# Kernel tuning notes

Measured on AMD Instinct MI355X. Metric: run time of the kernel, lower is better.

The kernel has to match this reference:

```python
import jax, jax.numpy as jnp
import numpy as np

GAMMA = 9.6
BETA = 0.83
LAMDA = 10.0
EPS = 1e-12

B, D, C = 1024, 512, 10000


def _l2norm(x):
    # torch F.normalize: x / max(||x||_2, eps)
    n = jnp.sqrt(jnp.sum(x * x, axis=1, keepdims=True))
    return x / jnp.maximum(n, EPS)


def setup_inputs() -> dict:
    key = jax.random.key(0)
    k1, k2, k3, k4 = jax.random.split(key, 4)
    inp = jax.random.normal(k1, (B, D), dtype=jnp.float32)
    # xavier-uniform-like init for the classifier weight
    limit = float(np.sqrt(6.0 / (C + D)))
    weight = jax.random.uniform(k2, (C, D), dtype=jnp.float32, minval=-limit, maxval=limit)
    class_weight = jax.random.uniform(k3, (C,), dtype=jnp.float32)  # per-class margins in [0,1)
    label = jax.random.randint(k4, (B,), 0, C, dtype=jnp.int32)
    return {"input": inp, "weight": weight, "class_weight": class_weight, "label": label}


def reference(input, weight, class_weight, label):
    x = _l2norm(input)            # [B, D]
    w = _l2norm(weight)           # [C, D]
    fea = x @ w.T                 # [B, C] cosine logits

    # sp_i = fea[i, label_i]; logit_{ij} = sn_ij - sp_i + beta * m_j  (j != label_i)
    sp = jnp.take_along_axis(fea, label[:, None], axis=1)           # [B, 1]
    logits = GAMMA * (fea - sp + BETA * class_weight[None, :])      # [B, C]
    pos_mask = label[:, None] == jnp.arange(C, dtype=label.dtype)[None, :]
    logits = jnp.where(pos_mask, -jnp.inf, logits)                  # drop positive column
    lse = jax.scipy.special.logsumexp(logits, axis=1)               # [B]
    loss = jax.nn.softplus(lse)                                     # [B]

    # inter-class similarity penalty
    score = jnp.clip(w @ w.T, -1.0, 1.0)                            # [C, C]
    score = score * (1.0 - jnp.eye(C, dtype=score.dtype))           # zero diagonal
    s = jnp.max(score[label], axis=1)                               # [B]
    loss_w = jax.nn.softplus(jnp.mean(s) + 0.5)

    loss = loss + LAMDA * loss_w
    return fea, jnp.mean(loss)
```

## Files before the change

### kernel.cpp

```cpp
#include <hip/hip_runtime.h>
#include <math.h>

#define GAMMA 9.6f
#define BETA  0.83f
#define LAMDA 10.0f
#define B_ 1024
#define D_ 512
#define C_ 10000
#define M0_ 20.0f

#define WS_XB   0
#define WS_WB   1048576
#define WS_SU   11288576
#define WS_T    11292672
#define WS_SP   11296768

typedef __attribute__((ext_vector_type(8))) short short8;
typedef __attribute__((ext_vector_type(4))) float floatx4;

__device__ __forceinline__ unsigned enc_f(float f) {
    unsigned i = __float_as_uint(f);
    return (i & 0x80000000u) ? ~i : (i | 0x80000000u);
}
__device__ __forceinline__ float dec_f(unsigned u) {
    return (u & 0x80000000u) ? __uint_as_float(u ^ 0x80000000u)
                             : __uint_as_float(~u);
}
__device__ __forceinline__ float softplus_f(float x) {
    return (x > 30.f) ? x : log1pf(expf(x));
}
__device__ __forceinline__ unsigned short f2bf_rne(float f) {
    unsigned u = __float_as_uint(f);
    u += 0x7FFFu + ((u >> 16) & 1u);
    return (unsigned short)(u >> 16);
}

__global__ __launch_bounds__(128) void normcvt_kernel(
    const float* __restrict__ input, const float* __restrict__ weight,
    unsigned short* __restrict__ xb, unsigned short* __restrict__ wb,
    unsigned* __restrict__ s_u, float* __restrict__ T) {
    int row = blockIdx.x;
    int tid = threadIdx.x;
    if (row < B_ && tid == 0) { s_u[row] = 0u; T[row] = 0.f; }

    const float* src = (row < B_) ? (input + (size_t)row * D_)
                                  : (weight + (size_t)(row - B_) * D_);
    float4 v = *(const float4*)(src + tid * 4);
    float ss = v.x * v.x + v.y * v.y + v.z * v.z + v.w * v.w;
    #pragma unroll
    for (int o = 32; o > 0; o >>= 1) ss += __shfl_xor(ss, o, 64);
    __shared__ float red[2];
    if ((tid & 63) == 0) red[tid >> 6] = ss;
    __syncthreads();
    float inv = 1.0f / fmaxf(sqrtf(red[0] + red[1]), 1e-12f);
    unsigned short* dst = (row < B_) ? (xb + (size_t)row * D_)
                                     : (wb + (size_t)(row - B_) * D_);
    ushort4 o4;
    o4.x = f2bf_rne(v.x * inv);
    o4.y = f2bf_rne(v.y * inv);
    o4.z = f2bf_rne(v.z * inv);
    o4.w = f2bf_rne(v.w * inv);
    *(ushort4*)(dst + tid * 4) = o4;
}

#define BM 128
#define BN 128
#define BK 64
#define NKT (D_ / BK)
#define NTILE_M 16
#define NTILE_N 79
#define NWG (NTILE_M * NTILE_N)

__global__ __launch_bounds__(256) void mfma_gemm_kernel(
    const unsigned short* __restrict__ xb, const unsigned short* __restrict__ wb,
    const int* __restrict__ label, const float* __restrict__ cw,
    float* __restrict__ fea, unsigned* __restrict__ s_u,
    float* __restrict__ T, float* __restrict__ sp) {
    __shared__ __align__(16) unsigned short As[2][2][128 * 32];
    __shared__ __align__(16) unsigned short Bs[2][2][128 * 32];

    const int tid = threadIdx.x;
    const int orig = (blockIdx.x & 7) * (NWG / 8) + (blockIdx.x >> 3);
    const int m0 = (orig & 15) * BM;
    const int n0 = (orig >> 4) * BN;
    const bool feaTile = (m0 < B_);

    const int srow = tid >> 2;
    const int kchunk = (tid & 3) ^ ((tid >> 3) & 3);
    const unsigned short* asrc[2];
    const unsigned short* bsrc[2];
    #pragma unroll
    for (int q = 0; q < 2; q++) {
        int rm = m0 + srow + q * 64;
        const unsigned short* ab;
        if (rm < B_) ab = xb + (size_t)rm * D_;
        else         ab = wb + (size_t)label[rm - B_] * D_;
        asrc[q] = ab + kchunk * 8;
        int rn = n0 + srow + q * 64;
        if (rn >= C_) rn = C_ - 1;
        bsrc[q] = wb + (size_t)rn * D_ + kchunk * 8;
    }

    const int lane = tid & 63;
    const int wv = tid >> 6;
    const int wr = (wv >> 1) * 64;
    const int wc = (wv & 1) * 64;
    const int l15 = lane & 15;
    const int hi = lane >> 4;
    const int xs = (l15 >> 1) & 3;

    floatx4 acc[4][4];
    #pragma unroll
    for (int i = 0; i < 4; i++)
        #pragma unroll
        for (int j = 0; j < 4; j++)
            acc[i][j] = (floatx4){0.f, 0.f, 0.f, 0.f};

#define STAGE(bufn, ksn, ktelem)                                               \
    {                                                                          \
        _Pragma("unroll")                                                      \
        for (int q = 0; q < 2; q++) {                                          \
            __builtin_amdgcn_global_load_lds(                                  \
                (const __attribute__((address_space(1))) void*)(asrc[q] + (ktelem)), \
                (__attribute__((address_space(3))) void*)((char*)&As[bufn][ksn][0] + (q * 256 + tid) * 16), \
                16, 0, 0);                                                     \
            __builtin_amdgcn_global_load_lds(                                  \
                (const __attribute__((address_space(1))) void*)(bsrc[q] + (ktelem)), \
                (__attribute__((address_space(3))) void*)((char*)&Bs[bufn][ksn][0] + (q * 256 + tid) * 16), \
                16, 0, 0);                                                     \
        }                                                                      \
    }

    STAGE(0, 0, 0);
    STAGE(0, 1, 32);

    #pragma unroll
    for (int t = 0; t < NKT; ++t) {
        const int cur = t & 1;
        #pragma unroll
        for (int ks = 0; ks < 2; ++ks) {
            if (t == NKT - 1 && ks == 1)
                asm volatile("s_waitcnt vmcnt(0)" ::: "memory");
            else
                asm volatile("s_waitcnt vmcnt(4)" ::: "memory");
            __builtin_amdgcn_s_barrier();
            __builtin_amdgcn_sched_barrier(0);

            short8 a[4], b[4];
            #pragma unroll
            for (int i = 0; i < 4; i++)
                a[i] = *(const short8*)&As[cur][ks]
                        [(wr + i * 16 + l15) * 32 + ((hi ^ xs) << 3)];
            #pragma unroll
            for (int j = 0; j < 4; j++)
                b[j] = *(const short8*)&Bs[cur][ks]
                        [(wc + j * 16 + l15) * 32 + ((hi ^ xs) << 3)];

            if (t + 1 < NKT) STAGE(cur ^ 1, ks, (t + 1) * 64 + ks * 32);

            __builtin_amdgcn_s_setprio(1);
            #pragma unroll
            for (int i = 0; i < 4; i++)
                #pragma unroll
                for (int j = 0; j < 4; j++)
                    acc[i][j] = __builtin_amdgcn_mfma_f32_16x16x32_bf16(
                        a[i], b[j], acc[i][j], 0, 0, 0);
            __builtin_amdgcn_s_setprio(0);
        }
    }

    if (feaTile) {
        int lbl_ir[4][4];
        #pragma unroll
        for (int i = 0; i < 4; i++)
            #pragma unroll
            for (int r = 0; r < 4; r++)
                lbl_ir[i][r] = label[m0 + wr + i * 16 + hi * 4 + r];
        float cwj[4];
        #pragma unroll
        for (int j = 0; j < 4; j++) {
            int n = n0 + wc + j * 16 + l15;
            cwj[j] = (n < C_) ? cw[n] : 0.f;
        }
        float rs[4][4];
        #pragma unroll
        for (int i = 0; i < 4; i++)
            #pragma unroll
            for (int r = 0; r < 4; r++) rs[i][r] = 0.f;

        #pragma unroll
        for (int i = 0; i < 4; i++) {
            #pragma unroll
            for (int j = 0; j < 4; j++) {
                int n = n0 + wc + j * 16 + l15;
                if (n < C_) {
                    int m = m0 + wr + i * 16 + hi * 4;
                    float* dst = fea + (size_t)m * C_ + n;
                    #pragma unroll
                    for (int r = 0; r < 4; r++) {
                        float v = acc[i][j][r];
                        dst[(size_t)r * C_] = v;
                        int l = lbl_ir[i][r];
                        if (n == l) sp[m + r] = v;
                        else rs[i][r] += expf(GAMMA * (v + BETA * cwj[j]) - M0_);
                    }
                }
            }
        }
        #pragma unroll
        for (int i = 0; i < 4; i++) {
            #pragma unroll
            for (int r = 0; r < 4; r++) {
                float s = rs[i][r];
                #pragma unroll
                for (int o = 8; o > 0; o >>= 1) s += __shfl_xor(s, o, 64);
                if (l15 == 0)
                    atomicAdd(T + (m0 + wr + i * 16 + hi * 4 + r), s);
            }
        }
    } else {
        #pragma unroll
        for (int i = 0; i < 4; i++) {
            #pragma unroll
            for (int r = 0; r < 4; r++) {
                int row = m0 - B_ + wr + i * 16 + hi * 4 + r;
                int l = label[row];
                float vmax = -2.f;
                #pragma unroll
                for (int j = 0; j < 4; j++) {
                    int n = n0 + wc + j * 16 + l15;
                    float v = fminf(fmaxf(acc[i][j][r], -1.f), 1.f);
                    if (n == l) v = 0.f;
                    if (n < C_) vmax = fmaxf(vmax, v);
                }
                #pragma unroll
                for (int o = 8; o > 0; o >>= 1)
                    vmax = fmaxf(vmax, __shfl_xor(vmax, o, 64));
                if (l15 == 0) atomicMax(s_u + row, enc_f(vmax));
            }
        }
    }
}

__global__ __launch_bounds__(1024) void final_kernel(
    const unsigned* __restrict__ s_u, const float* __restrict__ T,
    const float* __restrict__ sp, float* __restrict__ out_loss) {
    int tid = threadIdx.x;
    float lse = M0_ + logf(T[tid]) - GAMMA * sp[tid];
    float lr = softplus_f(lse);
    float sv = dec_f(s_u[tid]);
    #pragma unroll
    for (int o = 32; o > 0; o >>= 1) {
        lr += __shfl_xor(lr, o, 64);
        sv += __shfl_xor(sv, o, 64);
    }
    __shared__ float red_l[16], red_s[16];
    if ((tid & 63) == 0) { red_l[tid >> 6] = lr; red_s[tid >> 6] = sv; }
    __syncthreads();
    if (tid == 0) {
        float tl = 0.f, ts = 0.f;
        #pragma unroll
        for (int w = 0; w < 16; w++) { tl += red_l[w]; ts += red_s[w]; }
        float loss_w = softplus_f(ts / (float)B_ + 0.5f);
        *out_loss = tl / (float)B_ + LAMDA * loss_w;
    }
}

extern "C" void kernel_launch(void* const* d_in, const int* in_sizes, int n_in,
                              void* d_out, int out_size, void* d_ws, size_t ws_size,
                              hipStream_t stream) {
    const float* input  = (const float*)d_in[0];
    const float* weight = (const float*)d_in[1];
    const float* cw     = (const float*)d_in[2];
    const int*   label  = (const int*)d_in[3];
    float* out = (float*)d_out;

    char* ws = (char*)d_ws;
    unsigned short* xb = (unsigned short*)(ws + WS_XB);
    unsigned short* wb = (unsigned short*)(ws + WS_WB);
    unsigned* s_u      = (unsigned*)(ws + WS_SU);
    float*    T        = (float*)(ws + WS_T);
    float*    sp       = (float*)(ws + WS_SP);

    normcvt_kernel<<<B_ + C_, 128, 0, stream>>>(input, weight, xb, wb, s_u, T);

    mfma_gemm_kernel<<<NWG, 256, 0, stream>>>(xb, wb, label, cw, out, s_u, T, sp);

    final_kernel<<<1, 1024, 0, stream>>>(s_u, T, sp, out + (size_t)B_ * C_);
}
```

Before: 75.48 us.

## Enlarge GEMM tiles to 256x256 with 8 waves and staged K-split pipeline

Moves the fused GEMM from 128x128 tiles with 4 waves to 256x256 tiles with 8 waves (512 threads). Each wave now computes 128x64 outputs in two halves per K sub-step. The global-to-LDS loads are interleaved across four barrier-separated phases so prefetch overlaps MFMA work. The aim is more data reuse per loaded byte and fewer workgroups. In exchange, accumulator registers double, there are only 320 workgroups on the device, and the larger last tile wastes more N padding.

```diff
diff --git a/kernel.cpp b/kernel.cpp
--- a/kernel.cpp
+++ b/kernel.cpp
@@ -63,26 +63,26 @@
     *(ushort4*)(dst + tid * 4) = o4;
 }
 
-#define BM 128
-#define BN 128
+#define BM 256
+#define BN 256
 #define BK 64
 #define NKT (D_ / BK)
-#define NTILE_M 16
-#define NTILE_N 79
+#define NTILE_M 8
+#define NTILE_N 40
 #define NWG (NTILE_M * NTILE_N)
 
-__global__ __launch_bounds__(256) void mfma_gemm_kernel(
+__global__ __launch_bounds__(512) void mfma_gemm_kernel(
     const unsigned short* __restrict__ xb, const unsigned short* __restrict__ wb,
     const int* __restrict__ label, const float* __restrict__ cw,
     float* __restrict__ fea, unsigned* __restrict__ s_u,
     float* __restrict__ T, float* __restrict__ sp) {
-    __shared__ __align__(16) unsigned short As[2][2][128 * 32];
-    __shared__ __align__(16) unsigned short Bs[2][2][128 * 32];
+    __shared__ __align__(16) unsigned short As[2][2][2][128 * 32];
+    __shared__ __align__(16) unsigned short Bs[2][2][2][128 * 32];
 
     const int tid = threadIdx.x;
     const int orig = (blockIdx.x & 7) * (NWG / 8) + (blockIdx.x >> 3);
-    const int m0 = (orig & 15) * BM;
-    const int n0 = (orig >> 4) * BN;
+    const int m0 = (orig & 7) * BM;
+    const int n0 = (orig >> 3) * BN;
     const bool feaTile = (m0 < B_);
 
     const int srow = tid >> 2;
@@ -90,145 +90,164 @@
     const unsigned short* asrc[2];
     const unsigned short* bsrc[2];
     #pragma unroll
-    for (int q = 0; q < 2; q++) {
-        int rm = m0 + srow + q * 64;
+    for (int h = 0; h < 2; h++) {
+        int rm = m0 + h * 128 + srow;
         const unsigned short* ab;
         if (rm < B_) ab = xb + (size_t)rm * D_;
         else         ab = wb + (size_t)label[rm - B_] * D_;
-        asrc[q] = ab + kchunk * 8;
-        int rn = n0 + srow + q * 64;
+        asrc[h] = ab + kchunk * 8;
+        int rn = n0 + h * 128 + srow;
         if (rn >= C_) rn = C_ - 1;
-        bsrc[q] = wb + (size_t)rn * D_ + kchunk * 8;
+        bsrc[h] = wb + (size_t)rn * D_ + kchunk * 8;
     }
 
     const int lane = tid & 63;
-    const int wv = tid >> 6;
-    const int wr = (wv >> 1) * 64;
-    const int wc = (wv & 1) * 64;
+    const int wid = tid >> 6;
+    const int wm = wid >> 2;
+    const int wn = wid & 3;
+    const int wnh = wn >> 1;
+    const int wnl = (wn & 1) * 64;
     const int l15 = lane & 15;
     const int hi = lane >> 4;
     const int xs = (l15 >> 1) & 3;
 
-    floatx4 acc[4][4];
-    #pragma unroll
-    for (int i = 0; i < 4; i++)
+    floatx4 acc[8][4];
+    #pragma unroll
+    for (int i = 0; i < 8; i++)
         #pragma unroll
         for (int j = 0; j < 4; j++)
             acc[i][j] = (floatx4){0.f, 0.f, 0.f, 0.f};
 
-#define STAGE(bufn, ksn, ktelem)                                               \
-    {                                                                          \
-        _Pragma("unroll")                                                      \
-        for (int q = 0; q < 2; q++) {                                          \
-            __builtin_amdgcn_global_load_lds(                                  \
-                (const __attribute__((address_space(1))) void*)(asrc[q] + (ktelem)), \
-                (__attribute__((address_space(3))) void*)((char*)&As[bufn][ksn][0] + (q * 256 + tid) * 16), \
-                16, 0, 0);                                                     \
-            __builtin_amdgcn_global_load_lds(                                  \
-                (const __attribute__((address_space(1))) void*)(bsrc[q] + (ktelem)), \
-                (__attribute__((address_space(3))) void*)((char*)&Bs[bufn][ksn][0] + (q * 256 + tid) * 16), \
-                16, 0, 0);                                                     \
-        }                                                                      \
-    }
-
-    STAGE(0, 0, 0);
-    STAGE(0, 1, 32);
+#define STA(bufn, hh, ss, koff)                                                \
+    __builtin_amdgcn_global_load_lds(                                          \
+        (const __attribute__((address_space(1))) void*)(asrc[hh] + (koff)),    \
+        (__attribute__((address_space(3))) void*)((char*)&As[bufn][hh][ss][0] + tid * 16), \
+        16, 0, 0)
+#define STB(bufn, hh, ss, koff)                                                \
+    __builtin_amdgcn_global_load_lds(                                          \
+        (const __attribute__((address_space(1))) void*)(bsrc[hh] + (koff)),    \
+        (__attribute__((address_space(3))) void*)((char*)&Bs[bufn][hh][ss][0] + tid * 16), \
+        16, 0, 0)
+
+    STA(0, 0, 0, 0);  STA(0, 1, 0, 0);
+    STB(0, 0, 0, 0);  STB(0, 1, 0, 0);
+    STA(0, 0, 1, 32); STA(0, 1, 1, 32);
+    STB(0, 0, 1, 32); STB(0, 1, 1, 32);
+    STA(1, 0, 0, 64); STA(1, 1, 0, 64);
 
     #pragma unroll
     for (int t = 0; t < NKT; ++t) {
-        const int cur = t & 1;
-        #pragma unroll
-        for (int ks = 0; ks < 2; ++ks) {
-            if (t == NKT - 1 && ks == 1)
-                asm volatile("s_waitcnt vmcnt(0)" ::: "memory");
-            else
-                asm volatile("s_waitcnt vmcnt(4)" ::: "memory");
-            __builtin_amdgcn_s_barrier();
-            __builtin_amdgcn_sched_barrier(0);
-
-            short8 a[4], b[4];
-            #pragma unroll
-            for (int i = 0; i < 4; i++)
-                a[i] = *(const short8*)&As[cur][ks]
-                        [(wr + i * 16 + l15) * 32 + ((hi ^ xs) << 3)];
+        const int cur = t & 1, nxt = cur ^ 1;
+        const int kn = (t + 1) * BK;
+        short8 a[4], b[4];
+        if (t < NKT - 1) asm volatile("s_waitcnt vmcnt(2)" ::: "memory");
+        else             asm volatile("s_waitcnt vmcnt(0)" ::: "memory");
+        __builtin_amdgcn_s_barrier();
+        __builtin_amdgcn_sched_barrier(0);
+        #pragma unroll
+        for (int i = 0; i < 4; i++)
+            a[i] = *(const short8*)&As[cur][wm][0][((i * 16 + l15) << 5) + ((hi ^ xs) << 3)];
+        #pragma unroll
+        for (int j = 0; j < 4; j++)
+            b[j] = *(const short8*)&Bs[cur][wnh][0][((wnl + j * 16 + l15) << 5) + ((hi ^ xs) << 3)];
+        if (t < NKT - 1) { STB(nxt, 0, 0, kn); STB(nxt, 1, 0, kn); }
+        __builtin_amdgcn_s_setprio(1);
+        #pragma unroll
+        for (int i = 0; i < 4; i++)
             #pragma unroll
             for (int j = 0; j < 4; j++)
-                b[j] = *(const short8*)&Bs[cur][ks]
-                        [(wc + j * 16 + l15) * 32 + ((hi ^ xs) << 3)];
-
-            if (t + 1 < NKT) STAGE(cur ^ 1, ks, (t + 1) * 64 + ks * 32);
-
-            __builtin_amdgcn_s_setprio(1);
-            #pragma unroll
-            for (int i = 0; i < 4; i++)
-                #pragma unroll
-                for (int j = 0; j < 4; j++)
-                    acc[i][j] = __builtin_amdgcn_mfma_f32_16x16x32_bf16(
-                        a[i], b[j], acc[i][j], 0, 0, 0);
-            __builtin_amdgcn_s_setprio(0);
-        }
-    }
-
+                acc[i][j] = __builtin_amdgcn_mfma_f32_16x16x32_bf16(a[i], b[j], acc[i][j], 0, 0, 0);
+        __builtin_amdgcn_s_setprio(0);
+        __builtin_amdgcn_s_barrier();
+        #pragma unroll
+        for (int i = 0; i < 4; i++)
+            a[i] = *(const short8*)&As[cur][wm][0][(((i + 4) * 16 + l15) << 5) + ((hi ^ xs) << 3)];
+        if (t < NKT - 1) { STA(nxt, 0, 1, kn + 32); STA(nxt, 1, 1, kn + 32); }
+        __builtin_amdgcn_s_setprio(1);
+        #pragma unroll
+        for (int i = 0; i < 4; i++)
+            #pragma unroll
+            for (int j = 0; j < 4; j++)
+                acc[i + 4][j] = __builtin_amdgcn_mfma_f32_16x16x32_bf16(a[i], b[j], acc[i + 4][j], 0, 0, 0);
+        __builtin_amdgcn_s_setprio(0);
+        __builtin_amdgcn_s_barrier();
+        #pragma unroll
+        for (int i = 0; i < 4; i++)
+            a[i] = *(const short8*)&As[cur][wm][1][((i * 16 + l15) << 5) + ((hi ^ xs) << 3)];
+        #pragma unroll
+        for (int j = 0; j < 4; j++)
+            b[j] = *(const short8*)&Bs[cur][wnh][1][((wnl + j * 16 + l15) << 5) + ((hi ^ xs) << 3)];
+        if (t < NKT - 1) { STB(nxt, 0, 1, kn + 32); STB(nxt, 1, 1, kn + 32); }
+        __builtin_amdgcn_s_setprio(1);
+        #pragma unroll
+        for (int i = 0; i < 4; i++)
+            #pragma unroll
+            for (int j = 0; j < 4; j++)
+                acc[i][j] = __builtin_amdgcn_mfma_f32_16x16x32_bf16(a[i], b[j], acc[i][j], 0, 0, 0);
+        __builtin_amdgcn_s_setprio(0);
+        __builtin_amdgcn_s_barrier();
+        #pragma unroll
+        for (int i = 0; i < 4; i++)
+            a[i] = *(const short8*)&As[cur][wm][1][(((i + 4) * 16 + l15) << 5) + ((hi ^ xs) << 3)];
+        __builtin_amdgcn_s_setprio(1);
+        #pragma unroll
+        for (int i = 0; i < 4; i++)
+            #pragma unroll
+            for (int j = 0; j < 4; j++)
+                acc[i + 4][j] = __builtin_amdgcn_mfma_f32_16x16x32_bf16(a[i], b[j], acc[i + 4][j], 0, 0, 0);
+        __builtin_amdgcn_s_setprio(0);
+        __builtin_amdgcn_s_barrier();
+        __builtin_amdgcn_sched_barrier(0);
+        if (t < NKT - 2) { STA(cur, 0, 0, kn + 64); STA(cur, 1, 0, kn + 64); }
+    }
+
+    float cwj[4];
+    #pragma unroll
+    for (int j = 0; j < 4; j++) {
+        int n = n0 + wn * 64 + j * 16 + l15;
+        cwj[j] = (feaTile && n < C_) ? cw[n] : 0.f;
+    }
     if (feaTile) {
-        int lbl_ir[4][4];
-        #pragma unroll
-        for (int i = 0; i < 4; i++)
-            #pragma unroll
-            for (int r = 0; r < 4; r++)
-                lbl_ir[i][r] = label[m0 + wr + i * 16 + hi * 4 + r];
-        float cwj[4];
-        #pragma unroll
-        for (int j = 0; j < 4; j++) {
-            int n = n0 + wc + j * 16 + l15;
-            cwj[j] = (n < C_) ? cw[n] : 0.f;
-        }
-        float rs[4][4];
-        #pragma unroll
-        for (int i = 0; i < 4; i++)
-            #pragma unroll
-            for (int r = 0; r < 4; r++) rs[i][r] = 0.f;
-
-        #pragma unroll
-        for (int i = 0; i < 4; i++) {
+        #pragma unroll
+        for (int i = 0; i < 8; i++) {
+            int mbase = m0 + wm * 128 + i * 16 + hi * 4;
+            int lblr[4];
+            #pragma unroll
+            for (int r = 0; r < 4; r++) lblr[r] = label[mbase + r];
+            float rsr[4] = {0.f, 0.f, 0.f, 0.f};
             #pragma unroll
             for (int j = 0; j < 4; j++) {
-                int n = n0 + wc + j * 16 + l15;
+                int n = n0 + wn * 64 + j * 16 + l15;
                 if (n < C_) {
-                    int m = m0 + wr + i * 16 + hi * 4;
-                    float* dst = fea + (size_t)m * C_ + n;
+                    float* dst = fea + (size_t)mbase * C_ + n;
                     #pragma unroll
                     for (int r = 0; r < 4; r++) {
                         float v = acc[i][j][r];
                         dst[(size_t)r * C_] = v;
-                        int l = lbl_ir[i][r];
-                        if (n == l) sp[m + r] = v;
-                        else rs[i][r] += expf(GAMMA * (v + BETA * cwj[j]) - M0_);
+                        if (n == lblr[r]) sp[mbase + r] = v;
+                        else rsr[r] += expf(GAMMA * (v + BETA * cwj[j]) - M0_);
                     }
                 }
             }
-        }
-        #pragma unroll
-        for (int i = 0; i < 4; i++) {
             #pragma unroll
             for (int r = 0; r < 4; r++) {
-                float s = rs[i][r];
+                float s = rsr[r];
                 #pragma unroll
                 for (int o = 8; o > 0; o >>= 1) s += __shfl_xor(s, o, 64);
-                if (l15 == 0)
-                    atomicAdd(T + (m0 + wr + i * 16 + hi * 4 + r), s);
+                if (l15 == 0) atomicAdd(T + mbase + r, s);
             }
         }
     } else {
         #pragma unroll
-        for (int i = 0; i < 4; i++) {
+        for (int i = 0; i < 8; i++) {
+            int rbase = m0 - B_ + wm * 128 + i * 16 + hi * 4;
             #pragma unroll
             for (int r = 0; r < 4; r++) {
-                int row = m0 - B_ + wr + i * 16 + hi * 4 + r;
-                int l = label[row];
+                int l = label[rbase + r];
                 float vmax = -2.f;
                 #pragma unroll
                 for (int j = 0; j < 4; j++) {
-                    int n = n0 + wc + j * 16 + l15;
+                    int n = n0 + wn * 64 + j * 16 + l15;
                     float v = fminf(fmaxf(acc[i][j][r], -1.f), 1.f);
                     if (n == l) v = 0.f;
                     if (n < C_) vmax = fmaxf(vmax, v);
@@ -236,7 +255,7 @@
                 #pragma unroll
                 for (int o = 8; o > 0; o >>= 1)
                     vmax = fmaxf(vmax, __shfl_xor(vmax, o, 64));
-                if (l15 == 0) atomicMax(s_u + row, enc_f(vmax));
+                if (l15 == 0) atomicMax(s_u + rbase + r, enc_f(vmax));
             }
         }
     }
@@ -284,7 +303,7 @@
 
     normcvt_kernel<<<B_ + C_, 128, 0, stream>>>(input, weight, xb, wb, s_u, T);
 
-    mfma_gemm_kernel<<<NWG, 256, 0, stream>>>(xb, wb, label, cw, out, s_u, T, sp);
+    mfma_gemm_kernel<<<NWG, 512, 0, stream>>>(xb, wb, label, cw, out, s_u, T, sp);
 
     final_kernel<<<1, 1024, 0, stream>>>(s_u, T, sp, out + (size_t)B_ * C_);
 }
```

Measured after the change: 95.43 us. 1.26x slower.
